# Kernel optimization log

Measured on AMD Instinct MI355X. Metric: run time of the kernel, lower is better.

The kernel has to match this reference:

```python
import jax, jax.numpy as jnp
import numpy as np

B, T, D = 4, 2048, 1024
NH, HD = 8, 128          # query heads, head dim
HKV = NH // 2            # kv heads (GQA)
ROPE_DIMS = 16
MM = 4
LN_SCALE = 1.0 / np.sqrt(11 + 1)  # layer_idx=11
EPS_RMS = 1e-6


def setup_inputs() -> dict:
    key = jax.random.key(0)
    ks = jax.random.split(key, 10)
    d = D
    # realistic RoPE tables for ROPE_DIMS//2 = 8 frequency pairs
    inv_freq = 1.0 / (10000.0 ** (np.arange(ROPE_DIMS // 2) / (ROPE_DIMS // 2)))
    ang = np.arange(T)[:, None] * inv_freq[None, :]
    s = lambda fan: 1.0 / np.sqrt(fan)
    return {
        "x": jax.random.normal(ks[0], (B, T, d), jnp.float32),
        "rope_cos": jnp.asarray(np.cos(ang), jnp.float32),
        "rope_sin": jnp.asarray(np.sin(ang), jnp.float32),
        "wq": jax.random.normal(ks[1], (d, d), jnp.float32) * s(d),
        "wk": jax.random.normal(ks[2], (d // 2, d), jnp.float32) * s(d),
        "wv": jax.random.normal(ks[3], (d // 2, d), jnp.float32) * s(d),
        "wo": jax.random.normal(ks[4], (d, d), jnp.float32) * s(d),
        "wfc": jax.random.normal(ks[5], (d * MM, d), jnp.float32) * s(d),
        "wproj": jax.random.normal(ks[6], (d, d * MM), jnp.float32) * s(d * MM),
        "attn_scale": jnp.ones((d,), jnp.float32),
        "mlp_scale": jnp.ones((d,), jnp.float32),
        "q_gain": jnp.full((NH,), 5.0, jnp.float32),
    }


def _rmsnorm(x, eps):
    return x * jax.lax.rsqrt(jnp.mean(jnp.square(x), axis=-1, keepdims=True) + eps)


def _partial_rope(x, cos, sin):
    # x: [B, H, T, hd]; rotate first ROPE_DIMS dims (interleaved pairs)
    t = x.shape[2]
    xr, xp = x[..., :ROPE_DIMS], x[..., ROPE_DIMS:]
    x1, x2 = xr[..., 0::2], xr[..., 1::2]
    c = cos[:t][None, None]  # [1,1,T,8]
    s = sin[:t][None, None]
    o1 = x1 * c - x2 * s
    o2 = x2 * c + x1 * s
    rot = jnp.stack([o1, o2], axis=-1).reshape(*x.shape[:-1], ROPE_DIMS)
    return jnp.concatenate([rot, xp], axis=-1)


def reference(x, rope_cos, rope_sin, wq, wk, wv, wo, wfc, wproj,
              attn_scale, mlp_scale, q_gain):
    b, t, c = x.shape
    group = NH // HKV
    h = _rmsnorm(x, EPS_RMS) * LN_SCALE

    q = (h @ wq.T).reshape(b, t, NH, HD).transpose(0, 2, 1, 3)    # [B,NH,T,hd]
    k = (h @ wk.T).reshape(b, t, HKV, HD).transpose(0, 2, 1, 3)   # [B,HKV,T,hd]
    v = (h @ wv.T).reshape(b, t, HKV, HD).transpose(0, 2, 1, 3)

    # F.rms_norm default eps = machine epsilon of dtype
    eps_head = jnp.finfo(x.dtype).eps
    q = _rmsnorm(q, eps_head) * q_gain[None, :, None, None]
    k = _rmsnorm(k, eps_head)

    q = _partial_rope(q, rope_cos, rope_sin)
    k = _partial_rope(k, rope_cos, rope_sin)

    # GQA causal attention
    qg = q.reshape(b, HKV, group, t, HD)
    scale = 1.0 / np.sqrt(HD)
    scores = jnp.einsum('bhgqd,bhkd->bhgqk', qg, k) * scale
    causal = jnp.tril(jnp.ones((t, t), bool))
    scores = jnp.where(causal[None, None, None], scores, -jnp.inf)
    p = jax.nn.softmax(scores, axis=-1)
    a = jnp.einsum('bhgqk,bhkd->bhgqd', p, v)                     # [B,HKV,g,T,hd]

    y_g = a.transpose(0, 3, 1, 2, 4)                              # [B,T,HKV,g,hd]
    v_t = v.transpose(0, 2, 1, 3)                                 # [B,T,HKV,hd]
    vn = v_t / jnp.maximum(jnp.linalg.norm(v_t, axis=-1, keepdims=True), 1e-12)
    vn = vn[:, :, :, None, :]                                     # [B,T,HKV,1,hd]
    proj = jnp.sum(y_g * vn, axis=-1, keepdims=True) * vn
    y = (y_g - proj).reshape(b, t, c)

    x = x + attn_scale * (y @ wo.T)

    h2 = _rmsnorm(x, EPS_RMS) * LN_SCALE
    u = h2 @ wfc.T
    act = jnp.square(jnp.where(u >= 0, u, 0.5 * u))               # leaky_relu(0.5)^2
    x = x + mlp_scale * (act @ wproj.T)
    return x
```

## Files before the change

kernel.cpp:

```cpp
#include <hip/hip_runtime.h>
#include <cstdint>
#include <cstddef>


typedef unsigned short u16;
typedef __attribute__((ext_vector_type(8))) short bf16x8;
typedef __attribute__((ext_vector_type(4))) float f32x4;

#define LOG2E 1.4426950408889634f

__device__ __forceinline__ u16 f2bf(float f) {
  unsigned u = __float_as_uint(f);
  u += 0x7FFFu + ((u >> 16) & 1u);
  return (u16)(u >> 16);
}
__device__ __forceinline__ unsigned pack2(float a, float b) {
  return (unsigned)f2bf(a) | ((unsigned)f2bf(b) << 16);
}

#define GLD16(g, l) __builtin_amdgcn_global_load_lds(                          \
    (const __attribute__((address_space(1))) void*)(g),                        \
    (__attribute__((address_space(3))) void*)(l), 16, 0, 0)

__global__ __launch_bounds__(256) void cvt_bf16_k(const float4* __restrict__ in,
                                                  uint2* __restrict__ out, int n4) {
  int i = blockIdx.x * 256 + threadIdx.x;
  if (i < n4) {
    float4 v = in[i];
    uint2 o; o.x = pack2(v.x, v.y); o.y = pack2(v.z, v.w);
    out[i] = o;
  }
}

__global__ __launch_bounds__(256) void rmsnorm_row_k(const float* __restrict__ x,
                                                     u16* __restrict__ out,
                                                     float eps, float scale) {
  const int row = blockIdx.x;
  const int tid = threadIdx.x, lane = tid & 63, wid = tid >> 6;
  const float4 v = ((const float4*)(x + (size_t)row * 1024))[tid];
  float ss = v.x * v.x + v.y * v.y + v.z * v.z + v.w * v.w;
#pragma unroll
  for (int d = 1; d < 64; d <<= 1) ss += __shfl_xor(ss, d);
  __shared__ float wsum[4];
  __shared__ float rbc;
  if (lane == 0) wsum[wid] = ss;
  __syncthreads();
  if (tid == 0)
    rbc = rsqrtf((wsum[0] + wsum[1] + wsum[2] + wsum[3]) * (1.f / 1024.f) + eps) * scale;
  __syncthreads();
  const float r = rbc;
  uint2 o; o.x = pack2(v.x * r, v.y * r); o.y = pack2(v.z * r, v.w * r);
  ((uint2*)(out + (size_t)row * 1024))[tid] = o;
}

template <int ISQ>
__global__ __launch_bounds__(256) void headnorm_rope_k(
    const float* __restrict__ in, int rstride, int cbase,
    const float* __restrict__ cosT, const float* __restrict__ sinT,
    const float* __restrict__ gain, u16* __restrict__ out, int hshift, float ps) {
  const int id = blockIdx.x * 4 + (threadIdx.x >> 6);
  const int lane = threadIdx.x & 63;
  const int h = id & ((1 << hshift) - 1);
  const size_t bt = (size_t)(id >> hshift);
  const int t = (int)(bt & 2047);
  const float2 v = *(const float2*)(in + bt * rstride + cbase + h * 128 + lane * 2);
  float ss = v.x * v.x + v.y * v.y;
#pragma unroll
  for (int d = 1; d < 64; d <<= 1) ss += __shfl_xor(ss, d);
  const float r = rsqrtf(ss * (1.f / 128.f) + 1.1920928955078125e-7f);
  float g;
  if (ISQ) g = gain[h] * ps; else g = ps;
  float a = v.x * r * g, c2 = v.y * r * g;
  if (lane < 8) {
    const float c = cosT[t * 8 + lane], s = sinT[t * 8 + lane];
    const float o1 = a * c - c2 * s, o2 = c2 * c + a * s;
    a = o1; c2 = o2;
  }
  ((unsigned*)out)[(size_t)id * 64 + lane] = pack2(a, c2);
}

__global__ __launch_bounds__(256) void transpose_v_k(const float* __restrict__ qkv,
                                                     u16* __restrict__ vt) {
  __shared__ float tile[32][33];
  const int bk = blockIdx.y;
  const int t0 = (blockIdx.x & 63) * 32;
  const int h0 = (blockIdx.x >> 6) * 32;
  const int tx = threadIdx.x & 31, ty = threadIdx.x >> 5;
  const int b = bk >> 2, kvh = bk & 3;
#pragma unroll
  for (int r = 0; r < 4; ++r) {
    const int tt = t0 + ty + r * 8;
    tile[ty + r * 8][tx] =
        qkv[(size_t)(b * 2048 + tt) * 2048 + 1536 + kvh * 128 + h0 + tx];
  }
  __syncthreads();
#pragma unroll
  for (int r = 0; r < 4; ++r) {
    const int hh = h0 + ty + r * 8;
    vt[((size_t)bk * 128 + hh) * 2048 + t0 + tx] = f2bf(tile[tx][ty + r * 8]);
  }
}

__global__ __launch_bounds__(256) void vproj_k(const float* __restrict__ qkv,
                                               const float* __restrict__ y,
                                               u16* __restrict__ ybf) {
  const int id = blockIdx.x * 4 + (threadIdx.x >> 6);
  const int lane = threadIdx.x & 63;
  const int kvh = id & 3;
  const size_t bt = (size_t)(id >> 2);
  const float2 vv = *(const float2*)(qkv + bt * 2048 + 1536 + kvh * 128 + lane * 2);
  float ss = vv.x * vv.x + vv.y * vv.y;
#pragma unroll
  for (int d = 1; d < 64; d <<= 1) ss += __shfl_xor(ss, d);
  const float inv = 1.f / fmaxf(sqrtf(ss), 1e-12f);
  const float n1 = vv.x * inv, n2 = vv.y * inv;
#pragma unroll
  for (int g = 0; g < 2; ++g) {
    const size_t off = (bt * 8 + kvh * 2 + g) * 128 + lane * 2;
    float2 yy = *(const float2*)(y + off);
    float dt = yy.x * n1 + yy.y * n2;
#pragma unroll
    for (int d = 1; d < 64; d <<= 1) dt += __shfl_xor(dt, d);
    yy.x -= dt * n1; yy.y -= dt * n2;
    ((unsigned*)ybf)[off >> 1] = pack2(yy.x, yy.y);
  }
}

template <int MODE>
__global__ __launch_bounds__(512) void gemm8_k(
    const u16* __restrict__ A, const u16* __restrict__ B,
    float* __restrict__ C, u16* __restrict__ Cb,
    const float* __restrict__ res, const float* __restrict__ cscale,
    int M, int N, int K, int nbx) {
  __shared__ __align__(16) u16 lds[3 * 256 * 64 + 3 * 128 * 64];
  char* AsB = (char*)&lds[0];
  char* BsB = (char*)&lds[3 * 256 * 64];
  const int tid = threadIdx.x, lane = tid & 63, wid = tid >> 6;
  const int r15 = lane & 15, hi = lane >> 4;
  const int wr = wid >> 1, wc = wid & 1;
  const int cpx = gridDim.x >> 3;
  const int idx = (blockIdx.x & 7) * cpx + (blockIdx.x >> 3);
  const int by = idx / nbx, bx = idx - by * nbx;
  const int bm0 = by * 256, bn0 = bx * 128;
  const u16* Abase = A + (size_t)bm0 * K;
  const u16* Bbase = B + (size_t)bn0 * K;

  auto stageA4 = [&](int kt, int slot) {
#pragma unroll
    for (int it = 0; it < 4; ++it) {
      const int u = it * 512 + tid;
      const int row = u >> 3;
      const int c16 = (u & 7) ^ (row & 7);
      GLD16(Abase + (size_t)row * K + kt + c16 * 8,
            AsB + slot * 32768 + (it * 512 + wid * 64) * 16);
    }
  };
  auto stageB2 = [&](int kt, int slot) {
#pragma unroll
    for (int it = 0; it < 2; ++it) {
      const int u = it * 512 + tid;
      const int row = u >> 3;
      const int c16 = (u & 7) ^ (row & 7);
      GLD16(Bbase + (size_t)row * K + kt + c16 * 8,
            BsB + slot * 16384 + (it * 512 + wid * 64) * 16);
    }
  };

  f32x4 acc[4][4];
#pragma unroll
  for (int m = 0; m < 4; ++m)
#pragma unroll
    for (int n = 0; n < 4; ++n) acc[m][n] = f32x4{0.f, 0.f, 0.f, 0.f};

  const int nT = K >> 6;
  stageA4(0, 0); stageB2(0, 0);
  stageA4(64, 1); stageB2(64, 1);
  asm volatile("s_waitcnt vmcnt(6)" ::: "memory");
  __builtin_amdgcn_s_barrier();

  for (int c = 0; c < nT; ++c) {
    const int slot = c % 3;
    char* As = AsB + slot * 32768;
    char* Bs = BsB + slot * 16384;
    const int pf = c + 2;
    const int pslot = pf % 3;
    bf16x8 aF[4][2], bF[2][2];
#pragma unroll
    for (int m = 0; m < 4; ++m)
#pragma unroll
      for (int kc = 0; kc < 2; ++kc) {
        const int row = wr * 64 + m * 16 + r15;
        aF[m][kc] = *(const bf16x8*)(As + row * 128 +
                        ((kc * 64 + hi * 16) ^ ((row & 7) << 4)));
      }
#pragma unroll
    for (int n = 0; n < 2; ++n)
#pragma unroll
      for (int kc = 0; kc < 2; ++kc) {
        const int row = wc * 64 + n * 16 + r15;
        bF[n][kc] = *(const bf16x8*)(Bs + row * 128 +
                        ((kc * 64 + hi * 16) ^ ((row & 7) << 4)));
      }
    if (pf < nT) stageA4(pf * 64, pslot);
    __builtin_amdgcn_sched_barrier(0);
    __builtin_amdgcn_s_barrier();
    __builtin_amdgcn_s_setprio(1);
#pragma unroll
    for (int m = 0; m < 4; ++m)
#pragma unroll
      for (int n = 0; n < 2; ++n)
#pragma unroll
        for (int kc = 0; kc < 2; ++kc)
          acc[m][n] = __builtin_amdgcn_mfma_f32_16x16x32_bf16(aF[m][kc], bF[n][kc], acc[m][n], 0, 0, 0);
    __builtin_amdgcn_s_setprio(0);
    __builtin_amdgcn_sched_barrier(0);
    __builtin_amdgcn_s_barrier();
#pragma unroll
    for (int n = 0; n < 2; ++n)
#pragma unroll
      for (int kc = 0; kc < 2; ++kc) {
        const int row = wc * 64 + (n + 2) * 16 + r15;
        bF[n][kc] = *(const bf16x8*)(Bs + row * 128 +
                        ((kc * 64 + hi * 16) ^ ((row & 7) << 4)));
      }
    if (pf < nT) stageB2(pf * 64, pslot);
    __builtin_amdgcn_sched_barrier(0);
    __builtin_amdgcn_s_barrier();
    __builtin_amdgcn_s_setprio(1);
#pragma unroll
    for (int m = 0; m < 4; ++m)
#pragma unroll
      for (int n = 0; n < 2; ++n)
#pragma unroll
        for (int kc = 0; kc < 2; ++kc)
          acc[m][n + 2] = __builtin_amdgcn_mfma_f32_16x16x32_bf16(aF[m][kc], bF[n][kc], acc[m][n + 2], 0, 0, 0);
    __builtin_amdgcn_s_setprio(0);
    __builtin_amdgcn_sched_barrier(0);
    if (pf < nT)          asm volatile("s_waitcnt vmcnt(6)" ::: "memory");
    else if (c + 1 < nT)  asm volatile("s_waitcnt vmcnt(0)" ::: "memory");
    __builtin_amdgcn_s_barrier();
  }
#pragma unroll
  for (int m = 0; m < 4; ++m) {
#pragma unroll
    for (int n = 0; n < 4; ++n) {
      const int gc = bn0 + wc * 64 + n * 16 + r15;
#pragma unroll
      for (int j = 0; j < 4; ++j) {
        const int gr = bm0 + wr * 64 + m * 16 + hi * 4 + j;
        const size_t o = (size_t)gr * N + gc;
        const float v = acc[m][n][j];
        if (MODE == 0) {
          C[o] = v;
        } else if (MODE == 1) {
          C[o] = res[o] + cscale[gc] * v;
        } else {
          const float tq = v >= 0.f ? v : 0.5f * v;
          Cb[o] = f2bf(tq * tq);
        }
      }
    }
  }
}

__global__ __launch_bounds__(256) void attn_k(const u16* __restrict__ Q,
                                              const u16* __restrict__ Kr,
                                              const u16* __restrict__ Vt,
                                              float* __restrict__ Oo) {
  __shared__ __align__(16) u16 Ks[128 * 128];
  __shared__ __align__(16) u16 Vs[128 * 128];
  __shared__ __align__(16) u16 Ps[4][16 * 128];
  const int idx = (blockIdx.x & 7) * 64 + (blockIdx.x >> 3);
  const int bh = idx >> 4, p = idx & 15;
  const int b = bh >> 3, h = bh & 7, kvh = h >> 1;
  const int tid = threadIdx.x, lane = tid & 63, wid = tid >> 6;
  const int r15 = lane & 15, hi = lane >> 4;
  const int sw = (r15 & 7) << 4;
  char* KsB = (char*)&Ks[0];
  char* VsB = (char*)&Vs[0];
  char* PsB = (char*)&Ps[wid][0];

  for (int seg = 0; seg < 2; ++seg) {
    const int qt = seg ? 31 - p : p;
    const int qbase = qt * 64;
    const int qrow = qbase + wid * 16 + r15;
    bf16x8 qf[4];
    {
      const u16* qp = Q + ((size_t)(b * 2048 + qrow) * 8 + h) * 128 + hi * 8;
#pragma unroll
      for (int kc = 0; kc < 4; ++kc) qf[kc] = *(const bf16x8*)(qp + kc * 32);
    }
    f32x4 Oa[8];
#pragma unroll
    for (int nn = 0; nn < 8; ++nn) Oa[nn] = f32x4{0.f, 0.f, 0.f, 0.f};
    float mrun[4], lrun[4];
#pragma unroll
    for (int j = 0; j < 4; ++j) { mrun[j] = -__builtin_inff(); lrun[j] = 0.f; }
    const int njt = (qt + 2) >> 1;

    for (int jt = 0; jt < njt; ++jt) {
#pragma unroll
      for (int it = 0; it < 8; ++it) {
        const int c0 = it * 256 + wid * 64;
        const int c = c0 + lane;
        const int row = c >> 4;
        const int ch = (c & 15) ^ (row & 7);
        GLD16(Kr + ((size_t)(b * 2048 + jt * 128 + row) * 4 + kvh) * 128 + ch * 8,
              KsB + c0 * 16);
        GLD16(Vt + ((size_t)(b * 4 + kvh) * 128 + row) * 2048 + jt * 128 + ch * 8,
              VsB + c0 * 16);
      }
      __syncthreads();
      f32x4 S[8];
#pragma unroll
      for (int n = 0; n < 8; ++n) S[n] = f32x4{0.f, 0.f, 0.f, 0.f};
#pragma unroll
      for (int kc = 0; kc < 4; ++kc) {
#pragma unroll
        for (int n = 0; n < 8; ++n) {
          bf16x8 kf = *(const bf16x8*)(KsB + ((((n * 16 + r15) * 256) + kc * 64 + hi * 16) ^ sw));
          S[n] = __builtin_amdgcn_mfma_f32_16x16x32_bf16(qf[kc], kf, S[n], 0, 0, 0);
        }
      }
      if (jt == njt - 1) {
#pragma unroll
        for (int n = 0; n < 8; ++n) {
          const int col = jt * 128 + n * 16 + r15;
#pragma unroll
          for (int j = 0; j < 4; ++j) {
            const int row = qbase + wid * 16 + hi * 4 + j;
            if (col > row) S[n][j] = -__builtin_inff();
          }
        }
      }
      float mt[4], al[4], rs[4];
#pragma unroll
      for (int j = 0; j < 4; ++j) {
        mt[j] = fmaxf(fmaxf(S[0][j], S[1][j]), fmaxf(S[2][j], S[3][j]));
        mt[j] = fmaxf(mt[j], fmaxf(fmaxf(S[4][j], S[5][j]), fmaxf(S[6][j], S[7][j])));
      }
#pragma unroll
      for (int d = 1; d < 16; d <<= 1)
#pragma unroll
        for (int j = 0; j < 4; ++j) mt[j] = fmaxf(mt[j], __shfl_xor(mt[j], d));
#pragma unroll
      for (int j = 0; j < 4; ++j) {
        const float mn = fmaxf(mrun[j], mt[j]);
        al[j] = exp2f((mrun[j] - mn) * LOG2E);
        mrun[j] = mn;
        rs[j] = 0.f;
      }
#pragma unroll
      for (int n = 0; n < 8; ++n)
#pragma unroll
        for (int j = 0; j < 4; ++j) {
          const float pv = exp2f((S[n][j] - mrun[j]) * LOG2E);
          rs[j] += pv;
          const int prow = hi * 4 + j;
          *(u16*)(PsB + ((prow * 256 + (n * 16 + r15) * 2) ^ ((prow & 7) << 4))) = f2bf(pv);
        }
#pragma unroll
      for (int d = 1; d < 16; d <<= 1)
#pragma unroll
        for (int j = 0; j < 4; ++j) rs[j] += __shfl_xor(rs[j], d);
#pragma unroll
      for (int j = 0; j < 4; ++j) lrun[j] = lrun[j] * al[j] + rs[j];
#pragma unroll
      for (int nn = 0; nn < 8; ++nn)
#pragma unroll
        for (int j = 0; j < 4; ++j) Oa[nn][j] *= al[j];
      asm volatile("s_waitcnt lgkmcnt(0)" ::: "memory");
      __builtin_amdgcn_sched_barrier(0);
#pragma unroll
      for (int kc = 0; kc < 4; ++kc) {
        const bf16x8 pf = *(const bf16x8*)(PsB + (((r15 * 256) + kc * 64 + hi * 16) ^ sw));
#pragma unroll
        for (int nn = 0; nn < 8; ++nn) {
          bf16x8 vf = *(const bf16x8*)(VsB + ((((nn * 16 + r15) * 256) + kc * 64 + hi * 16) ^ sw));
          Oa[nn] = __builtin_amdgcn_mfma_f32_16x16x32_bf16(pf, vf, Oa[nn], 0, 0, 0);
        }
      }
      __syncthreads();
    }
    float inv[4];
#pragma unroll
    for (int j = 0; j < 4; ++j) inv[j] = 1.f / lrun[j];
#pragma unroll
    for (int nn = 0; nn < 8; ++nn)
#pragma unroll
      for (int j = 0; j < 4; ++j) {
        const int row = qbase + wid * 16 + hi * 4 + j;
        Oo[((size_t)(b * 2048 + row) * 8 + h) * 128 + nn * 16 + r15] = Oa[nn][j] * inv[j];
      }
  }
}

extern "C" void kernel_launch(void* const* d_in, const int* in_sizes, int n_in,
                              void* d_out, int out_size, void* d_ws, size_t ws_size,
                              hipStream_t stream) {
  (void)in_sizes; (void)n_in; (void)out_size; (void)ws_size;
  const float* x          = (const float*)d_in[0];
  const float* rope_cos   = (const float*)d_in[1];
  const float* rope_sin   = (const float*)d_in[2];
  const float* wq         = (const float*)d_in[3];
  const float* wk         = (const float*)d_in[4];
  const float* wv         = (const float*)d_in[5];
  const float* wo         = (const float*)d_in[6];
  const float* wfc        = (const float*)d_in[7];
  const float* wproj      = (const float*)d_in[8];
  const float* attn_scale = (const float*)d_in[9];
  const float* mlp_scale  = (const float*)d_in[10];
  const float* q_gain     = (const float*)d_in[11];

  char* ws = (char*)d_ws;
  size_t off = 0;
  auto alloc = [&](size_t bytes) -> char* {
    char* p = ws + off;
    off += (bytes + 255) & ~(size_t)255;
    return p;
  };
  const size_t BT = 8192;
  u16*   h      = (u16*)alloc(BT * 1024 * 2);
  u16*   wqkv   = (u16*)alloc((size_t)2048 * 1024 * 2);
  u16*   wob    = (u16*)alloc((size_t)1024 * 1024 * 2);
  u16*   wfcb   = (u16*)alloc((size_t)4096 * 1024 * 2);
  u16*   wprojb = (u16*)alloc((size_t)1024 * 4096 * 2);
  float* qkv    = (float*)alloc(BT * 2048 * 4);
  u16*   qr     = (u16*)alloc(BT * 1024 * 2);
  u16*   krr    = (u16*)alloc(BT * 512 * 2);
  u16*   vt     = (u16*)alloc((size_t)16 * 128 * 2048 * 2);
  float* yg     = (float*)alloc(BT * 1024 * 4);
  u16*   ybf    = (u16*)alloc(BT * 1024 * 2);
  float* x2     = (float*)alloc(BT * 1024 * 4);
  u16*   actb   = (u16*)qkv;
  u16*   h2     = h;

  auto cvt = [&](const float* src, u16* dst, int n) {
    int n4 = n / 4;
    cvt_bf16_k<<<(n4 + 255) / 256, 256, 0, stream>>>((const float4*)src, (uint2*)dst, n4);
  };
  cvt(wq, wqkv, 1024 * 1024);
  cvt(wk, wqkv + (size_t)1024 * 1024, 512 * 1024);
  cvt(wv, wqkv + (size_t)1536 * 1024, 512 * 1024);
  cvt(wo, wob, 1024 * 1024);
  cvt(wfc, wfcb, 4096 * 1024);
  cvt(wproj, wprojb, 1024 * 4096);

  rmsnorm_row_k<<<8192, 256, 0, stream>>>(x, h, 1e-6f, 0.28867513459481287f);
  gemm8_k<0><<<512, 512, 0, stream>>>(h, wqkv, qkv, (u16*)nullptr,
                                      nullptr, nullptr, 8192, 2048, 1024, 16);
  headnorm_rope_k<1><<<16384, 256, 0, stream>>>(qkv, 2048, 0, rope_cos, rope_sin,
                                                q_gain, qr, 3, 0.08838834764831845f);
  headnorm_rope_k<0><<<8192, 256, 0, stream>>>(qkv, 2048, 1024, rope_cos, rope_sin,
                                               nullptr, krr, 2, 1.0f);
  transpose_v_k<<<dim3(256, 16), 256, 0, stream>>>(qkv, vt);
  attn_k<<<512, 256, 0, stream>>>(qr, krr, vt, yg);
  vproj_k<<<8192, 256, 0, stream>>>(qkv, yg, ybf);
  gemm8_k<1><<<256, 512, 0, stream>>>(ybf, wob, x2, nullptr,
                                      x, attn_scale, 8192, 1024, 1024, 8);
  rmsnorm_row_k<<<8192, 256, 0, stream>>>(x2, h2, 1e-6f, 0.28867513459481287f);
  gemm8_k<2><<<1024, 512, 0, stream>>>(h2, wfcb, nullptr, actb,
                                       nullptr, nullptr, 8192, 4096, 1024, 32);
  gemm8_k<1><<<256, 512, 0, stream>>>(actb, wprojb, (float*)d_out, nullptr,
                                      x2, mlp_scale, 8192, 1024, 4096, 8);
}
```

Before: 553.1 us.

## Double-buffer 64-key attention tiles and merge conversion and head-norm launches

The attention kernel now works on 64-key K/V tiles held in two LDS buffers, issuing the global-to-LDS loads for the next tile before computing on the current one. The smaller tiles also trim causal work on the diagonal, at the cost of more loop iterations and more barriers. Separately, the six weight-conversion launches become one kernel and the Q/K head-norm+RoPE launches become one kernel, cutting launch overhead. The merged conversion writes one contiguous output range and so assumes the bf16 weight buffers sit back-to-back in the workspace.

```diff
diff --git a/kernel.cpp b/kernel.cpp
--- a/kernel.cpp
+++ b/kernel.cpp
@@ -22,14 +22,22 @@
     (const __attribute__((address_space(1))) void*)(g),                        \
     (__attribute__((address_space(3))) void*)(l), 16, 0, 0)
 
-__global__ __launch_bounds__(256) void cvt_bf16_k(const float4* __restrict__ in,
-                                                  uint2* __restrict__ out, int n4) {
-  int i = blockIdx.x * 256 + threadIdx.x;
-  if (i < n4) {
-    float4 v = in[i];
-    uint2 o; o.x = pack2(v.x, v.y); o.y = pack2(v.z, v.w);
-    out[i] = o;
-  }
+__global__ __launch_bounds__(256) void cvt_all_k(
+    const float4* __restrict__ wq, const float4* __restrict__ wk,
+    const float4* __restrict__ wv, const float4* __restrict__ wo,
+    const float4* __restrict__ wfc, const float4* __restrict__ wproj,
+    uint2* __restrict__ out) {
+  const int i = blockIdx.x * 256 + threadIdx.x;
+  const float4* src; int local;
+  if (i < 262144)       { src = wq;    local = i; }
+  else if (i < 393216)  { src = wk;    local = i - 262144; }
+  else if (i < 524288)  { src = wv;    local = i - 393216; }
+  else if (i < 786432)  { src = wo;    local = i - 524288; }
+  else if (i < 1835008) { src = wfc;   local = i - 786432; }
+  else                  { src = wproj; local = i - 1835008; }
+  const float4 v = src[local];
+  uint2 o; o.x = pack2(v.x, v.y); o.y = pack2(v.z, v.w);
+  out[i] = o;
 }
 
 __global__ __launch_bounds__(256) void rmsnorm_row_k(const float* __restrict__ x,
@@ -53,30 +61,33 @@
   ((uint2*)(out + (size_t)row * 1024))[tid] = o;
 }
 
-template <int ISQ>
 __global__ __launch_bounds__(256) void headnorm_rope_k(
-    const float* __restrict__ in, int rstride, int cbase,
-    const float* __restrict__ cosT, const float* __restrict__ sinT,
-    const float* __restrict__ gain, u16* __restrict__ out, int hshift, float ps) {
-  const int id = blockIdx.x * 4 + (threadIdx.x >> 6);
+    const float* __restrict__ qkv, const float* __restrict__ cosT,
+    const float* __restrict__ sinT, const float* __restrict__ gain,
+    u16* __restrict__ qr, u16* __restrict__ krr) {
+  const int id0 = blockIdx.x * 4 + (threadIdx.x >> 6);
   const int lane = threadIdx.x & 63;
+  const bool isq = id0 < 65536;
+  const int id = isq ? id0 : id0 - 65536;
+  const int hshift = isq ? 3 : 2;
   const int h = id & ((1 << hshift) - 1);
   const size_t bt = (size_t)(id >> hshift);
   const int t = (int)(bt & 2047);
-  const float2 v = *(const float2*)(in + bt * rstride + cbase + h * 128 + lane * 2);
+  const int cbase = isq ? 0 : 1024;
+  const float2 v = *(const float2*)(qkv + bt * 2048 + cbase + h * 128 + lane * 2);
   float ss = v.x * v.x + v.y * v.y;
 #pragma unroll
   for (int d = 1; d < 64; d <<= 1) ss += __shfl_xor(ss, d);
   const float r = rsqrtf(ss * (1.f / 128.f) + 1.1920928955078125e-7f);
-  float g;
-  if (ISQ) g = gain[h] * ps; else g = ps;
+  const float g = isq ? gain[h] * 0.08838834764831845f : 1.0f;
   float a = v.x * r * g, c2 = v.y * r * g;
   if (lane < 8) {
     const float c = cosT[t * 8 + lane], s = sinT[t * 8 + lane];
     const float o1 = a * c - c2 * s, o2 = c2 * c + a * s;
     a = o1; c2 = o2;
   }
-  ((unsigned*)out)[(size_t)id * 64 + lane] = pack2(a, c2);
+  unsigned* out = (unsigned*)(isq ? qr : krr);
+  out[(size_t)id * 64 + lane] = pack2(a, c2);
 }
 
 __global__ __launch_bounds__(256) void transpose_v_k(const float* __restrict__ qkv,
@@ -267,9 +278,9 @@
                                               const u16* __restrict__ Kr,
                                               const u16* __restrict__ Vt,
                                               float* __restrict__ Oo) {
-  __shared__ __align__(16) u16 Ks[128 * 128];
-  __shared__ __align__(16) u16 Vs[128 * 128];
-  __shared__ __align__(16) u16 Ps[4][16 * 128];
+  __shared__ __align__(16) u16 Ks[2 * 64 * 128];
+  __shared__ __align__(16) u16 Vs[2 * 128 * 64];
+  __shared__ __align__(16) u16 Ps[4][16 * 64];
   const int idx = (blockIdx.x & 7) * 64 + (blockIdx.x >> 3);
   const int bh = idx >> 4, p = idx & 15;
   const int b = bh >> 3, h = bh & 7, kvh = h >> 1;
@@ -279,6 +290,26 @@
   char* KsB = (char*)&Ks[0];
   char* VsB = (char*)&Vs[0];
   char* PsB = (char*)&Ps[wid][0];
+  const u16* KrB = Kr + (size_t)b * 2048 * 512 + kvh * 128;
+  const u16* VtB = Vt + ((size_t)(b * 4 + kvh) * 128) * 2048;
+
+  auto stageKV = [&](int jt, int buf) {
+#pragma unroll
+    for (int it = 0; it < 4; ++it) {
+      const int c0 = it * 256 + wid * 64;
+      const int c = c0 + lane;
+      {
+        const int row = c >> 4, ch = (c & 15) ^ (row & 7);
+        GLD16(KrB + (size_t)(jt * 64 + row) * 512 + ch * 8,
+              KsB + buf * 16384 + c0 * 16);
+      }
+      {
+        const int row = c >> 3, ch = (c & 7) ^ (row & 7);
+        GLD16(VtB + (size_t)row * 2048 + jt * 64 + ch * 8,
+              VsB + buf * 16384 + c0 * 16);
+      }
+    }
+  };
 
   for (int seg = 0; seg < 2; ++seg) {
     const int qt = seg ? 31 - p : p;
@@ -296,36 +327,33 @@
     float mrun[4], lrun[4];
 #pragma unroll
     for (int j = 0; j < 4; ++j) { mrun[j] = -__builtin_inff(); lrun[j] = 0.f; }
-    const int njt = (qt + 2) >> 1;
+    const int njt = qt + 1;
+
+    stageKV(0, 0);
+    asm volatile("s_waitcnt vmcnt(0)" ::: "memory");
+    __builtin_amdgcn_s_barrier();
+    int buf = 0;
 
     for (int jt = 0; jt < njt; ++jt) {
-#pragma unroll
-      for (int it = 0; it < 8; ++it) {
-        const int c0 = it * 256 + wid * 64;
-        const int c = c0 + lane;
-        const int row = c >> 4;
-        const int ch = (c & 15) ^ (row & 7);
-        GLD16(Kr + ((size_t)(b * 2048 + jt * 128 + row) * 4 + kvh) * 128 + ch * 8,
-              KsB + c0 * 16);
-        GLD16(Vt + ((size_t)(b * 4 + kvh) * 128 + row) * 2048 + jt * 128 + ch * 8,
-              VsB + c0 * 16);
-      }
-      __syncthreads();
-      f32x4 S[8];
-#pragma unroll
-      for (int n = 0; n < 8; ++n) S[n] = f32x4{0.f, 0.f, 0.f, 0.f};
+      if (jt + 1 < njt) stageKV(jt + 1, buf ^ 1);
+      __builtin_amdgcn_sched_barrier(0);
+      const int kvoff = buf * 16384;
+      f32x4 S[4];
+#pragma unroll
+      for (int n = 0; n < 4; ++n) S[n] = f32x4{0.f, 0.f, 0.f, 0.f};
 #pragma unroll
       for (int kc = 0; kc < 4; ++kc) {
 #pragma unroll
-        for (int n = 0; n < 8; ++n) {
-          bf16x8 kf = *(const bf16x8*)(KsB + ((((n * 16 + r15) * 256) + kc * 64 + hi * 16) ^ sw));
+        for (int n = 0; n < 4; ++n) {
+          bf16x8 kf = *(const bf16x8*)(KsB + kvoff +
+                          (((n * 16 + r15) * 256) + ((kc * 64 + hi * 16) ^ sw)));
           S[n] = __builtin_amdgcn_mfma_f32_16x16x32_bf16(qf[kc], kf, S[n], 0, 0, 0);
         }
       }
       if (jt == njt - 1) {
 #pragma unroll
-        for (int n = 0; n < 8; ++n) {
-          const int col = jt * 128 + n * 16 + r15;
+        for (int n = 0; n < 4; ++n) {
+          const int col = jt * 64 + n * 16 + r15;
 #pragma unroll
           for (int j = 0; j < 4; ++j) {
             const int row = qbase + wid * 16 + hi * 4 + j;
@@ -335,10 +363,8 @@
       }
       float mt[4], al[4], rs[4];
 #pragma unroll
-      for (int j = 0; j < 4; ++j) {
+      for (int j = 0; j < 4; ++j)
         mt[j] = fmaxf(fmaxf(S[0][j], S[1][j]), fmaxf(S[2][j], S[3][j]));
-        mt[j] = fmaxf(mt[j], fmaxf(fmaxf(S[4][j], S[5][j]), fmaxf(S[6][j], S[7][j])));
-      }
 #pragma unroll
       for (int d = 1; d < 16; d <<= 1)
 #pragma unroll
@@ -351,13 +377,13 @@
         rs[j] = 0.f;
       }
 #pragma unroll
-      for (int n = 0; n < 8; ++n)
+      for (int n = 0; n < 4; ++n)
 #pragma unroll
         for (int j = 0; j < 4; ++j) {
           const float pv = exp2f((S[n][j] - mrun[j]) * LOG2E);
           rs[j] += pv;
           const int prow = hi * 4 + j;
-          *(u16*)(PsB + ((prow * 256 + (n * 16 + r15) * 2) ^ ((prow & 7) << 4))) = f2bf(pv);
+          *(u16*)(PsB + ((prow * 128 + (n * 16 + r15) * 2) ^ ((prow & 7) << 4))) = f2bf(pv);
         }
 #pragma unroll
       for (int d = 1; d < 16; d <<= 1)
@@ -372,15 +398,18 @@
       asm volatile("s_waitcnt lgkmcnt(0)" ::: "memory");
       __builtin_amdgcn_sched_barrier(0);
 #pragma unroll
-      for (int kc = 0; kc < 4; ++kc) {
-        const bf16x8 pf = *(const bf16x8*)(PsB + (((r15 * 256) + kc * 64 + hi * 16) ^ sw));
+      for (int kc = 0; kc < 2; ++kc) {
+        const bf16x8 pf = *(const bf16x8*)(PsB + ((r15 * 128) + ((kc * 64 + hi * 16) ^ sw)));
 #pragma unroll
         for (int nn = 0; nn < 8; ++nn) {
-          bf16x8 vf = *(const bf16x8*)(VsB + ((((nn * 16 + r15) * 256) + kc * 64 + hi * 16) ^ sw));
+          bf16x8 vf = *(const bf16x8*)(VsB + kvoff +
+                          (((nn * 16 + r15) * 128) + ((kc * 64 + hi * 16) ^ sw)));
           Oa[nn] = __builtin_amdgcn_mfma_f32_16x16x32_bf16(pf, vf, Oa[nn], 0, 0, 0);
         }
       }
-      __syncthreads();
+      asm volatile("s_waitcnt vmcnt(0)" ::: "memory");
+      __builtin_amdgcn_s_barrier();
+      buf ^= 1;
     }
     float inv[4];
 #pragma unroll
@@ -435,24 +464,15 @@
   u16*   actb   = (u16*)qkv;
   u16*   h2     = h;
 
-  auto cvt = [&](const float* src, u16* dst, int n) {
-    int n4 = n / 4;
-    cvt_bf16_k<<<(n4 + 255) / 256, 256, 0, stream>>>((const float4*)src, (uint2*)dst, n4);
-  };
-  cvt(wq, wqkv, 1024 * 1024);
-  cvt(wk, wqkv + (size_t)1024 * 1024, 512 * 1024);
-  cvt(wv, wqkv + (size_t)1536 * 1024, 512 * 1024);
-  cvt(wo, wob, 1024 * 1024);
-  cvt(wfc, wfcb, 4096 * 1024);
-  cvt(wproj, wprojb, 1024 * 4096);
+  cvt_all_k<<<11264, 256, 0, stream>>>(
+      (const float4*)wq, (const float4*)wk, (const float4*)wv,
+      (const float4*)wo, (const float4*)wfc, (const float4*)wproj,
+      (uint2*)wqkv);
 
   rmsnorm_row_k<<<8192, 256, 0, stream>>>(x, h, 1e-6f, 0.28867513459481287f);
   gemm8_k<0><<<512, 512, 0, stream>>>(h, wqkv, qkv, (u16*)nullptr,
                                       nullptr, nullptr, 8192, 2048, 1024, 16);
-  headnorm_rope_k<1><<<16384, 256, 0, stream>>>(qkv, 2048, 0, rope_cos, rope_sin,
-                                                q_gain, qr, 3, 0.08838834764831845f);
-  headnorm_rope_k<0><<<8192, 256, 0, stream>>>(qkv, 2048, 1024, rope_cos, rope_sin,
-                                               nullptr, krr, 2, 1.0f);
+  headnorm_rope_k<<<24576, 256, 0, stream>>>(qkv, rope_cos, rope_sin, q_gain, qr, krr);
   transpose_v_k<<<dim3(256, 16), 256, 0, stream>>>(qkv, vt);
   attn_k<<<512, 256, 0, stream>>>(qr, krr, vt, yg);
   vproj_k<<<8192, 256, 0, stream>>>(qkv, yg, ybf);
```

After: 499.4 us. -9.7%, faster.
